# Optimization experiments

Measured on AMD Instinct MI355X. Metric: run time of the kernel, lower is better.

The kernel has to match this reference:

```python
import jax, jax.numpy as jnp
import numpy as np

B, V, DIN, DOUT, S = 32768, 43, 64, 64, 2  # batch, local_graph_vert=43, dims, n_supports


def setup_inputs() -> dict:
    key = jax.random.key(0)
    k1, k2, k3 = jax.random.split(key, 3)
    x = jax.random.normal(k1, (B, V, DIN), dtype=jnp.float32)
    adj = jax.random.uniform(k2, (S, V, V), dtype=jnp.float32)
    # glorot init per support weight matrix
    scale = jnp.sqrt(6.0 / (DIN + DOUT)).astype(jnp.float32)
    W = jax.random.uniform(k3, (S, DIN, DOUT), minval=-1.0, maxval=1.0, dtype=jnp.float32) * scale
    b = jnp.zeros((DOUT,), dtype=jnp.float32)
    return {"x": x, "adj": adj, "W": W, "b": b}


def reference(x, adj, W, b):
    # For each support s: pre_s = x @ W_s  (einsum 'bvi,sio->sbvo')
    #                     out += adj_s @ pre_s  (einsum 'suv,sbvo->buo')
    # Fused multi-support reduction in one einsum; dropout rate is 0 (dropout=False).
    out = jnp.einsum('suv,bvi,sio->buo', adj, x, W)  # [B, V, DOUT]
    out = out + b
    return jax.nn.relu(out)
```

## Files before the change

### kernel.cpp

```cpp
#include <hip/hip_runtime.h>
#include <stdint.h>


#define BATCH 32768
#define NV 43
#define DIN 64
#define DOUT 64
#define NS 2

#define PSTRIDE 72
#define ASTRIDE 72
#define NWAVES 4

typedef __attribute__((ext_vector_type(8))) short short8;
typedef __attribute__((ext_vector_type(4))) float f32x4;
typedef __attribute__((ext_vector_type(4))) unsigned short ushort4_t;

__device__ __forceinline__ unsigned short f2bf(float f) {
    union { float f; unsigned int u; } x;
    x.f = f;
    unsigned int r = x.u + 0x7FFFu + ((x.u >> 16) & 1u);
    return (unsigned short)(r >> 16);
}

__global__ void __launch_bounds__(256, 2) lgconv_kernel(
    const float* __restrict__ xg,
    const float* __restrict__ adjg,
    const float* __restrict__ wg,
    const float* __restrict__ bg,
    float* __restrict__ outg)
{
    __shared__ __align__(16) unsigned short s_adj[NS * 48 * ASTRIDE];
    __shared__ __align__(16) unsigned short s_pre[NWAVES * 64 * PSTRIDE];

    const int tid  = threadIdx.x;
    const int wave = tid >> 6;
    const int lane = tid & 63;
    const int quad = lane >> 4;
    const int l16  = lane & 15;

    for (int t = tid; t < NS * DIN * DOUT; t += 256)
        s_pre[t] = f2bf(wg[t]);
    __syncthreads();

    short8 wfrag[NS][2][4];
    for (int s = 0; s < NS; ++s)
      for (int kc = 0; kc < 2; ++kc)
        for (int nt = 0; nt < 4; ++nt) {
          short8 f;
          #pragma unroll
          for (int j = 0; j < 8; ++j) {
            int i = kc * 32 + quad * 8 + j;
            f[j] = (short)s_pre[(s * DIN + i) * DOUT + nt * 16 + l16];
          }
          wfrag[s][kc][nt] = f;
        }
    float biasv[4];
    #pragma unroll
    for (int nt = 0; nt < 4; ++nt) biasv[nt] = bg[nt * 16 + l16];
    __syncthreads();

    for (int t = tid; t < NWAVES * 64 * PSTRIDE; t += 256) s_pre[t] = 0;
    for (int t = tid; t < NS * 48 * ASTRIDE; t += 256) s_adj[t] = 0;
    __syncthreads();
    for (int t = tid; t < NS * NV * NV; t += 256) {
        int s  = t / (NV * NV);
        int rc = t - s * NV * NV;
        int r  = rc / NV;
        int c  = rc - r * NV;
        s_adj[(s * 48 + r) * ASTRIDE + c] = f2bf(adjg[t]);
    }
    __syncthreads();

    unsigned short* mypre = &s_pre[wave * 64 * PSTRIDE];
    const int gwave = blockIdx.x * NWAVES + wave;
    const int nwv   = gridDim.x * NWAVES;

    for (int b = gwave; b < BATCH; b += nwv) {
        short8 afrag[3][2];
        #pragma unroll
        for (int mt = 0; mt < 3; ++mt) {
            int m = mt * 16 + l16;
            bool valid = (m < NV);
            const float* p = xg + ((size_t)b * NV + m) * DIN + quad * 8;
            #pragma unroll
            for (int kc = 0; kc < 2; ++kc) {
                f32x4 u0 = {0.f, 0.f, 0.f, 0.f};
                f32x4 u1 = {0.f, 0.f, 0.f, 0.f};
                if (valid) {
                    u0 = *(const f32x4*)(p + kc * 32);
                    u1 = *(const f32x4*)(p + kc * 32 + 4);
                }
                short8 f;
                f[0] = (short)f2bf(u0[0]); f[1] = (short)f2bf(u0[1]);
                f[2] = (short)f2bf(u0[2]); f[3] = (short)f2bf(u0[3]);
                f[4] = (short)f2bf(u1[0]); f[5] = (short)f2bf(u1[1]);
                f[6] = (short)f2bf(u1[2]); f[7] = (short)f2bf(u1[3]);
                afrag[mt][kc] = f;
            }
        }

        f32x4 oacc[3][4];
        #pragma unroll
        for (int mt = 0; mt < 3; ++mt)
            #pragma unroll
            for (int nt = 0; nt < 4; ++nt)
                oacc[mt][nt] = (f32x4){0.f, 0.f, 0.f, 0.f};

        #pragma unroll
        for (int s = 0; s < NS; ++s) {
            #pragma unroll
            for (int mt = 0; mt < 3; ++mt) {
                #pragma unroll
                for (int nt = 0; nt < 4; ++nt) {
                    f32x4 c = (f32x4){0.f, 0.f, 0.f, 0.f};
                    c = __builtin_amdgcn_mfma_f32_16x16x32_bf16(afrag[mt][0], wfrag[s][0][nt], c, 0, 0, 0);
                    c = __builtin_amdgcn_mfma_f32_16x16x32_bf16(afrag[mt][1], wfrag[s][1][nt], c, 0, 0, 0);
                    ushort4_t pk;
                    pk[0] = f2bf(c[0]); pk[1] = f2bf(c[1]);
                    pk[2] = f2bf(c[2]); pk[3] = f2bf(c[3]);
                    int o  = nt * 16 + l16;
                    int v0 = mt * 16 + quad * 4;
                    *(ushort4_t*)(mypre + o * PSTRIDE + v0) = pk;
                }
            }
            __builtin_amdgcn_s_waitcnt(0xc07f);

            #pragma unroll
            for (int kc = 0; kc < 2; ++kc) {
                short8 bfr[4];
                #pragma unroll
                for (int nt = 0; nt < 4; ++nt)
                    bfr[nt] = *(const short8*)(mypre + (nt * 16 + l16) * PSTRIDE + kc * 32 + quad * 8);
                #pragma unroll
                for (int mt = 0; mt < 3; ++mt) {
                    short8 afr = *(const short8*)(&s_adj[(s * 48 + mt * 16 + l16) * ASTRIDE + kc * 32 + quad * 8]);
                    #pragma unroll
                    for (int nt = 0; nt < 4; ++nt)
                        oacc[mt][nt] = __builtin_amdgcn_mfma_f32_16x16x32_bf16(afr, bfr[nt], oacc[mt][nt], 0, 0, 0);
                }
            }
        }

        size_t obase = (size_t)b * (NV * DOUT);
        #pragma unroll
        for (int mt = 0; mt < 3; ++mt) {
            #pragma unroll
            for (int r = 0; r < 4; ++r) {
                int u = mt * 16 + quad * 4 + r;
                if (u < NV) {
                    #pragma unroll
                    for (int nt = 0; nt < 4; ++nt) {
                        float vv = oacc[mt][nt][r] + biasv[nt];
                        vv = fmaxf(vv, 0.0f);
                        outg[obase + (size_t)u * DOUT + nt * 16 + l16] = vv;
                    }
                }
            }
        }
    }
}

extern "C" void kernel_launch(void* const* d_in, const int* in_sizes, int n_in,
                              void* d_out, int out_size, void* d_ws, size_t ws_size,
                              hipStream_t stream) {
    (void)in_sizes; (void)n_in; (void)d_ws; (void)ws_size; (void)out_size;
    const float* xg   = (const float*)d_in[0];
    const float* adjg = (const float*)d_in[1];
    const float* wg   = (const float*)d_in[2];
    const float* bg   = (const float*)d_in[3];
    float* outg = (float*)d_out;

    dim3 grid(1024), block(256);
    hipLaunchKernelGGL(lgconv_kernel, grid, block, 0, stream, xg, adjg, wg, bg, outg);
}
```

Measured before the change: 597.8 us.

## Software-prefetch next batch's x rows and use packed bf16 conversion

Loads for the next batch element are issued into registers right after converting the current one, so global-memory latency overlaps with the MFMA work. The manual bf16 rounding is replaced with the packed float2-to-bfloat162 intrinsic, and invalid rows are clamped rather than branched. The grid is halved to 512 blocks, which doubles the batch elements each wave handles. The prefetch buffer costs extra registers and could hurt occupancy, and the smaller grid may leave some CUs underused.

Measured after the change: 599.6 us. About the same (+0.3%).

```diff
diff --git a/kernel.cpp b/kernel.cpp
--- a/kernel.cpp
+++ b/kernel.cpp
@@ -1,4 +1,5 @@
 #include <hip/hip_runtime.h>
+#include <hip/hip_bf16.h>
 #include <stdint.h>
 
 
@@ -14,13 +15,38 @@
 
 typedef __attribute__((ext_vector_type(8))) short short8;
 typedef __attribute__((ext_vector_type(4))) float f32x4;
-typedef __attribute__((ext_vector_type(4))) unsigned short ushort4_t;
+typedef __attribute__((ext_vector_type(2))) unsigned int uint2_t;
+
+union U8 { short8 s8; unsigned int u[4]; };
 
 __device__ __forceinline__ unsigned short f2bf(float f) {
     union { float f; unsigned int u; } x;
     x.f = f;
     unsigned int r = x.u + 0x7FFFu + ((x.u >> 16) & 1u);
     return (unsigned short)(r >> 16);
+}
+
+__device__ __forceinline__ unsigned int pk2bf(float a, float b) {
+    __hip_bfloat162 h2 = __float22bfloat162_rn(make_float2(a, b));
+    unsigned int u;
+    __builtin_memcpy(&u, &h2, 4);
+    return u;
+}
+
+__device__ __forceinline__ void issue_loads(const float* __restrict__ xg, int b,
+                                            f32x4 L[3][2][2], int l16, int quad) {
+    const float* pb = xg + (size_t)b * (NV * DIN);
+    #pragma unroll
+    for (int mt = 0; mt < 3; ++mt) {
+        int m = mt * 16 + l16;
+        if (m > NV - 1) m = NV - 1;
+        const float* p = pb + m * DIN + quad * 8;
+        #pragma unroll
+        for (int kc = 0; kc < 2; ++kc) {
+            L[mt][kc][0] = *(const f32x4*)(p + kc * 32);
+            L[mt][kc][1] = *(const f32x4*)(p + kc * 32 + 4);
+        }
+    }
 }
 
 __global__ void __launch_bounds__(256, 2) lgconv_kernel(
@@ -76,29 +102,28 @@
     const int gwave = blockIdx.x * NWAVES + wave;
     const int nwv   = gridDim.x * NWAVES;
 
+    f32x4 L[3][2][2];
+    issue_loads(xg, gwave, L, l16, quad);
+
     for (int b = gwave; b < BATCH; b += nwv) {
         short8 afrag[3][2];
         #pragma unroll
         for (int mt = 0; mt < 3; ++mt) {
-            int m = mt * 16 + l16;
-            bool valid = (m < NV);
-            const float* p = xg + ((size_t)b * NV + m) * DIN + quad * 8;
+            bool valid = (mt * 16 + l16 < NV);
             #pragma unroll
             for (int kc = 0; kc < 2; ++kc) {
-                f32x4 u0 = {0.f, 0.f, 0.f, 0.f};
-                f32x4 u1 = {0.f, 0.f, 0.f, 0.f};
-                if (valid) {
-                    u0 = *(const f32x4*)(p + kc * 32);
-                    u1 = *(const f32x4*)(p + kc * 32 + 4);
-                }
-                short8 f;
-                f[0] = (short)f2bf(u0[0]); f[1] = (short)f2bf(u0[1]);
-                f[2] = (short)f2bf(u0[2]); f[3] = (short)f2bf(u0[3]);
-                f[4] = (short)f2bf(u1[0]); f[5] = (short)f2bf(u1[1]);
-                f[6] = (short)f2bf(u1[2]); f[7] = (short)f2bf(u1[3]);
-                afrag[mt][kc] = f;
-            }
-        }
+                U8 ff;
+                ff.u[0] = pk2bf(L[mt][kc][0][0], L[mt][kc][0][1]);
+                ff.u[1] = pk2bf(L[mt][kc][0][2], L[mt][kc][0][3]);
+                ff.u[2] = pk2bf(L[mt][kc][1][0], L[mt][kc][1][1]);
+                ff.u[3] = pk2bf(L[mt][kc][1][2], L[mt][kc][1][3]);
+                if (!valid) { ff.u[0] = 0; ff.u[1] = 0; ff.u[2] = 0; ff.u[3] = 0; }
+                afrag[mt][kc] = ff.s8;
+            }
+        }
+
+        int bn = b + nwv;
+        issue_loads(xg, (bn < BATCH) ? bn : b, L, l16, quad);
 
         f32x4 oacc[3][4];
         #pragma unroll
@@ -116,12 +141,12 @@
                     f32x4 c = (f32x4){0.f, 0.f, 0.f, 0.f};
                     c = __builtin_amdgcn_mfma_f32_16x16x32_bf16(afrag[mt][0], wfrag[s][0][nt], c, 0, 0, 0);
                     c = __builtin_amdgcn_mfma_f32_16x16x32_bf16(afrag[mt][1], wfrag[s][1][nt], c, 0, 0, 0);
-                    ushort4_t pk;
-                    pk[0] = f2bf(c[0]); pk[1] = f2bf(c[1]);
-                    pk[2] = f2bf(c[2]); pk[3] = f2bf(c[3]);
+                    uint2_t pk;
+                    pk[0] = pk2bf(c[0], c[1]);
+                    pk[1] = pk2bf(c[2], c[3]);
                     int o  = nt * 16 + l16;
                     int v0 = mt * 16 + quad * 4;
-                    *(ushort4_t*)(mypre + o * PSTRIDE + v0) = pk;
+                    *(uint2_t*)(mypre + o * PSTRIDE + v0) = pk;
                 }
             }
             __builtin_amdgcn_s_waitcnt(0xc07f);
@@ -171,6 +196,6 @@
     const float* bg   = (const float*)d_in[3];
     float* outg = (float*)d_out;
 
-    dim3 grid(1024), block(256);
+    dim3 grid(512), block(256);
     hipLaunchKernelGGL(lgconv_kernel, grid, block, 0, stream, xg, adjg, wg, bg, outg);
 }
```
